# Kernel tuning notes

Measured on AMD Instinct MI355X. Metric: run time of the kernel, lower is better.

Reference implementation:

```python
import jax, jax.numpy as jnp
import numpy as np

N_IN = 1024
H = 16
N_QK = 64
N_V = 64
T = 2048
B = 2


def setup_inputs() -> dict:
    key = jax.random.key(0)
    ks = jax.random.split(key, 7)
    s = 1.0 / np.sqrt(N_IN)
    return {
        "x": jax.random.normal(ks[0], (T, B, N_IN), dtype=jnp.float32),
        "mask": jnp.ones((B, T), dtype=bool),
        "Wk": jax.random.normal(ks[1], (H * N_QK, N_IN), dtype=jnp.float32) * s,
        "bk": jax.random.normal(ks[2], (H * N_QK,), dtype=jnp.float32) * s,
        "Wq": jax.random.normal(ks[3], (H * N_QK, N_IN), dtype=jnp.float32) * s,
        "bq": jax.random.normal(ks[4], (H * N_QK,), dtype=jnp.float32) * s,
        "Wv": jax.random.normal(ks[5], (H * N_V, N_IN), dtype=jnp.float32) * s,
        "bv": jax.random.normal(ks[6], (H * N_V,), dtype=jnp.float32) * s,
    }


def reference(x, mask, Wk, bk, Wq, bq, Wv, bv):
    # x: (T, B, N_in); mask: (B, T) bool
    keys = (x @ Wk.T + bk).reshape(T, B, H, N_QK)      # (T,B,h,n_qk)
    queries = (x @ Wq.T + bq).reshape(T, B, H, N_QK)
    # kern[b,h,i,k] = keys_i . queries_k / sqrt(N_in)  (scale uses N_in, as in source)
    kern = jnp.einsum('ibhj,kbhj->bhik', keys, queries) / np.sqrt(N_IN)
    kern = jnp.where(mask[:, None, None, :], kern, -jnp.inf)
    A = jax.nn.softmax(kern, axis=-1)                  # softmax over last (query-index) axis
    values = (x @ Wv.T + bv).reshape(T, B, H, N_V)     # (T,B,h,n_v)
    out = jnp.einsum('bhij,jbhk->ibhk', A, values)     # (T,B,h,n_v)
    return out.reshape(T, B, H * N_V)
```

## Files before the change

kernel.cpp:

```cpp
#include <hip/hip_runtime.h>
#include <hip/hip_bf16.h>

#define TT 2048
#define BB 2
#define HH 16
#define DD 64
#define NIN 1024

#define KSCALE 0.0450842218f

using bf16x8 = __attribute__((ext_vector_type(8))) short;
using f32x4  = __attribute__((ext_vector_type(4))) float;
using f32x16 = __attribute__((ext_vector_type(16))) float;

__device__ __forceinline__ short f2b(float f) {
  union { float fl; unsigned u; } v; v.fl = f;
  return (short)((v.u + 0x7FFFu + ((v.u >> 16) & 1u)) >> 16);
}

__device__ __forceinline__ float exp2_fast(float x) {
  float r;
  asm("v_exp_f32 %0, %1" : "=v"(r) : "v"(x));
  return r;
}

__device__ __forceinline__ unsigned cvtpk(float lo, float hi) {
  unsigned r;
  asm("v_cvt_pk_bf16_f32 %0, %1, %2" : "=v"(r) : "v"(lo), "v"(hi));
  return r;
}

__device__ __forceinline__ void gld_lds16(const void* g, void* lds) {
  __builtin_amdgcn_global_load_lds(
      (const __attribute__((address_space(1))) void*)g,
      (__attribute__((address_space(3))) void*)lds, 16, 0, 0);
}

__global__ void cast_all_k(const float* __restrict__ x, const float* __restrict__ wk,
                           const float* __restrict__ wq, const float* __restrict__ wv,
                           short* __restrict__ xbf, short* __restrict__ wall) {
  int i = blockIdx.x * 256 + threadIdx.x;
  float4 v;
  short4* dp;
  float sc;
  if (i < 1048576) {
    v = reinterpret_cast<const float4*>(x)[i];
    dp = reinterpret_cast<short4*>(xbf) + i;
    sc = 1.0f;
  } else {
    int j = i - 1048576;
    int seg = j >> 18;
    const float* w = seg == 0 ? wk : (seg == 1 ? wq : wv);
    sc = (seg == 0) ? KSCALE : 1.0f;
    v = reinterpret_cast<const float4*>(w)[j & 262143];
    dp = reinterpret_cast<short4*>(wall) + j;
  }
  short4 o;
  o.x = f2b(v.x * sc);
  o.y = f2b(v.y * sc);
  o.z = f2b(v.z * sc);
  o.w = f2b(v.w * sc);
  *dp = o;
}

__device__ __forceinline__ int permc(int c) {
  return (c & 64) | ((c & 15) << 2) | ((c >> 4) & 3);
}

__global__ __launch_bounds__(256, 3)
void proj_gemm_k(const short* __restrict__ X, const short* __restrict__ Wall,
                 const float* __restrict__ bk, const float* __restrict__ bq,
                 const float* __restrict__ bv,
                 short* __restrict__ Kb, short* __restrict__ Qb, short* __restrict__ Vb) {
  __shared__ short As[128][64];
  __shared__ short Bs[128][64];
  const int tid = threadIdx.x;
  const int w = tid >> 6, l = tid & 63;
  const int bm = blockIdx.x, bn = blockIdx.y;
  const int wr = (w >> 1) * 64, wc = (w & 1) * 64;

  f32x4 acc[4][4] = {};
  const int sr = w * 8 + (l >> 3);

  for (int kt = 0; kt < NIN / 64; ++kt) {
    __syncthreads();
#pragma unroll
    for (int it = 0; it < 4; ++it) {
      int row = it * 32 + sr;
      int gc = ((l & 7) ^ (row & 7)) << 3;
      gld_lds16(X + (size_t)(bm * 128 + row) * NIN + kt * 64 + gc, &As[it * 32 + w * 8][0]);
      gld_lds16(Wall + (size_t)(bn * 128 + permc(row)) * NIN + kt * 64 + gc, &Bs[it * 32 + w * 8][0]);
    }
    __syncthreads();
#pragma unroll
    for (int kk = 0; kk < 2; ++kk) {
      bf16x8 af[4], bfr[4];
#pragma unroll
      for (int mf = 0; mf < 4; ++mf) {
        int row = wr + mf * 16 + (l & 15);
        af[mf] = *(const bf16x8*)&As[row][(kk * 32 + (l >> 4) * 8) ^ ((row & 7) << 3)];
      }
#pragma unroll
      for (int nf = 0; nf < 4; ++nf) {
        int row = wc + nf * 16 + (l & 15);
        bfr[nf] = *(const bf16x8*)&Bs[row][(kk * 32 + (l >> 4) * 8) ^ ((row & 7) << 3)];
      }
#pragma unroll
      for (int mf = 0; mf < 4; ++mf)
#pragma unroll
        for (int nf = 0; nf < 4; ++nf)
          acc[mf][nf] = __builtin_amdgcn_mfma_f32_16x16x32_bf16(af[mf], bfr[nf], acc[mf][nf], 0, 0, 0);
    }
  }

  const int seg = bn >> 3;
  const float* bp = (seg == 0) ? bk : (seg == 1) ? bq : bv;
  const float bscale = (seg == 0) ? KSCALE : 1.0f;

  const int dbase = ((l & 15) << 2);
  const int h = ((bn << 1) | (wc >> 6)) & 15;
  float bsc[4];
#pragma unroll
  for (int nf = 0; nf < 4; ++nf) bsc[nf] = bp[h * 64 + dbase + nf] * bscale;

  if (seg < 2) {
    short* dst = (seg == 0) ? Kb : Qb;
#pragma unroll
    for (int mf = 0; mf < 4; ++mf) {
#pragma unroll
      for (int r = 0; r < 4; ++r) {
        int m = bm * 128 + wr + mf * 16 + (l >> 4) * 4 + r;
        int t = m >> 1, b = m & 1;
        short4 o4;
        o4.x = f2b(acc[mf][0][r] + bsc[0]);
        o4.y = f2b(acc[mf][1][r] + bsc[1]);
        o4.z = f2b(acc[mf][2][r] + bsc[2]);
        o4.w = f2b(acc[mf][3][r] + bsc[3]);
        *(short4*)&dst[(((size_t)(b * HH + h)) * TT + t) * DD + dbase] = o4;
      }
    }
  } else {
#pragma unroll
    for (int mf = 0; mf < 4; ++mf) {
#pragma unroll
      for (int nf = 0; nf < 4; ++nf) {
        int d = dbase + nf;
#pragma unroll
        for (int r = 0; r < 4; ++r) {
          int m = bm * 128 + wr + mf * 16 + (l >> 4) * 4 + r;
          short ov = f2b(acc[mf][nf][r] + bsc[nf]);
          int t = m >> 1, b = m & 1;
          int tp = (t & ~12) | ((t & 4) << 1) | ((t & 8) >> 1);
          Vb[(((size_t)(b * HH + h)) * DD + d) * TT + tp] = ov;
        }
      }
    }
  }
}

__global__ __launch_bounds__(256, 2)
void attn_k(const short* __restrict__ Kb, const short* __restrict__ Qb,
            const short* __restrict__ Vt, float* __restrict__ out) {
  __shared__ short smem[16384];
  short* QsB = smem;
  short* VsB = smem + 8192;

  const int tid = threadIdx.x;
  const int w = tid >> 6, l = tid & 63;
  const int hi = l >> 5;

  const int fid = blockIdx.x;
  const int nf_id = (fid & 7) * 64 + (fid >> 3);
  const int ib = nf_id & 15;
  const int bh = nf_id >> 4;
  const size_t base = (size_t)bh * TT * DD;

  const int sr = w * 8 + (l >> 3);
  const int gsw = l & 7;

  bf16x8 kf[4];
  {
    const short* kp = Kb + base + (size_t)(ib * 128 + w * 32 + (l & 31)) * DD + hi * 8;
#pragma unroll
    for (int kd = 0; kd < 4; ++kd)
      kf[kd] = *(const bf16x8*)(kp + kd * 16);
  }

#pragma unroll
  for (int it = 0; it < 2; ++it) {
    int row = it * 32 + sr;
    int gc = (gsw ^ (row & 7)) << 3;
    gld_lds16(Qb + base + (size_t)row * DD + gc, QsB + (it * 32 + w * 8) * 64);
    gld_lds16(Vt + base + (size_t)row * TT + gc, VsB + (it * 32 + w * 8) * 64);
  }
  __syncthreads();

  f32x16 oacc[2] = {};
  float lsum_p = 0.f;

  for (int jt = 0; jt < TT / 64; ++jt) {
    const int cur = jt & 1;
    const short* Qs = QsB + cur * 4096;
    const short* Vs = VsB + cur * 4096;

    if (jt + 1 < TT / 64) {
#pragma unroll
      for (int it = 0; it < 2; ++it) {
        int row = it * 32 + sr;
        int gc = (gsw ^ (row & 7)) << 3;
        gld_lds16(Qb + base + (size_t)((jt + 1) * 64 + row) * DD + gc,
                  QsB + (cur ^ 1) * 4096 + (it * 32 + w * 8) * 64);
        gld_lds16(Vt + base + (size_t)row * TT + (jt + 1) * 64 + gc,
                  VsB + (cur ^ 1) * 4096 + (it * 32 + w * 8) * 64);
      }
    }

    f32x16 sacc[2] = {};
    __builtin_amdgcn_s_setprio(1);
#pragma unroll
    for (int js = 0; js < 2; ++js) {
      int qrow = js * 32 + (l & 31);
#pragma unroll
      for (int kd = 0; kd < 4; ++kd) {
        bf16x8 qf = *(const bf16x8*)&Qs[qrow * 64 + ((kd * 16 + hi * 8) ^ ((qrow & 7) << 3))];
        sacc[js] = __builtin_amdgcn_mfma_f32_32x32x16_bf16(qf, kf[kd], sacc[js], 0, 0, 0);
      }
    }
    __builtin_amdgcn_s_setprio(0);

#pragma unroll
    for (int js = 0; js < 2; ++js)
#pragma unroll
      for (int t = 0; t < 16; ++t)
        sacc[js][t] = exp2_fast(sacc[js][t]);

    {
      float tsum[16];
#pragma unroll
      for (int t = 0; t < 16; ++t) tsum[t] = sacc[0][t] + sacc[1][t];
#pragma unroll
      for (int st = 8; st > 0; st >>= 1)
#pragma unroll
        for (int t = 0; t < st; ++t) tsum[t] += tsum[t + st];
      lsum_p += tsum[0];
    }

#pragma unroll
    for (int kd4 = 0; kd4 < 4; ++kd4) {
      const int js = kd4 >> 1;
      const int r0 = (kd4 & 1) * 8;
      union { unsigned u[4]; bf16x8 v; } pu;
      pu.u[0] = cvtpk(sacc[js][r0 + 0], sacc[js][r0 + 1]);
      pu.u[1] = cvtpk(sacc[js][r0 + 2], sacc[js][r0 + 3]);
      pu.u[2] = cvtpk(sacc[js][r0 + 4], sacc[js][r0 + 5]);
      pu.u[3] = cvtpk(sacc[js][r0 + 6], sacc[js][r0 + 7]);
      __builtin_amdgcn_s_setprio(1);
#pragma unroll
      for (int ds = 0; ds < 2; ++ds) {
        int vrow = ds * 32 + (l & 31);
        bf16x8 vf = *(const bf16x8*)&Vs[vrow * 64 + ((kd4 * 16 + hi * 8) ^ ((vrow & 7) << 3))];
        oacc[ds] = __builtin_amdgcn_mfma_f32_32x32x16_bf16(vf, pu.v, oacc[ds], 0, 0, 0);
      }
      __builtin_amdgcn_s_setprio(0);
    }

    __syncthreads();
  }

  const int b = bh >> 4, h = bh & 15;
  const float lsum = lsum_p + __shfl_xor(lsum_p, 32, 64);
  const float invl = 1.0f / lsum;
  const int i = ib * 128 + w * 32 + (l & 31);
  float* orow = out + ((size_t)i * BB + b) * (HH * DD) + h * DD;
#pragma unroll
  for (int ds = 0; ds < 2; ++ds)
#pragma unroll
    for (int g = 0; g < 4; ++g) {
      float4 t;
      t.x = oacc[ds][4 * g + 0] * invl;
      t.y = oacc[ds][4 * g + 1] * invl;
      t.z = oacc[ds][4 * g + 2] * invl;
      t.w = oacc[ds][4 * g + 3] * invl;
      *(float4*)(orow + ds * 32 + g * 8 + 4 * hi) = t;
    }
}

extern "C" void kernel_launch(void* const* d_in, const int* in_sizes, int n_in,
                              void* d_out, int out_size, void* d_ws, size_t ws_size,
                              hipStream_t stream) {
  const float* x  = (const float*)d_in[0];
  const float* Wk = (const float*)d_in[2];
  const float* bk = (const float*)d_in[3];
  const float* Wq = (const float*)d_in[4];
  const float* bq = (const float*)d_in[5];
  const float* Wv = (const float*)d_in[6];
  const float* bv = (const float*)d_in[7];
  float* out = (float*)d_out;

  char* ws = (char*)d_ws;
  short* Xbf  = (short*)(ws + 0);
  short* Wall = (short*)(ws + 8388608);
  short* Kb   = (short*)(ws + 14680064);
  short* Qb   = (short*)(ws + 23068672);
  short* Vb   = (short*)(ws + 31457280);

  cast_all_k<<<7168, 256, 0, stream>>>(x, Wk, Wq, Wv, Xbf, Wall);

  dim3 pg(32, 24);
  proj_gemm_k<<<pg, 256, 0, stream>>>(Xbf, Wall, bk, bq, bv, Kb, Qb, Vb);

  attn_k<<<512, 256, 0, stream>>>(Kb, Qb, Vb, out);
}
```

Before: 84.45 us.

## Replace LDS-staged attention with single-wave blocks loading Q/V directly to registers

The attention kernel drops shared-memory staging and the block-wide barriers. It now launches 2048 single-wavefront blocks, each handling 32 rows. Q and V fragments are read straight from global memory into registers, with Q double-buffered across a two-step unrolled loop so the next tile's loads overlap the current tile's MFMAs. This removes LDS traffic and __syncthreads, but each wave now loads Q/V independently, so there is no sharing across the 4 waves and global/L2 traffic is roughly four times higher. V loads are issued in the same iteration they are consumed, which can expose latency.

```diff
diff --git a/kernel.cpp b/kernel.cpp
--- a/kernel.cpp
+++ b/kernel.cpp
@@ -158,119 +158,114 @@
   }
 }
 
-__global__ __launch_bounds__(256, 2)
+__global__ __launch_bounds__(64, 2)
 void attn_k(const short* __restrict__ Kb, const short* __restrict__ Qb,
             const short* __restrict__ Vt, float* __restrict__ out) {
-  __shared__ short smem[16384];
-  short* QsB = smem;
-  short* VsB = smem + 8192;
-
-  const int tid = threadIdx.x;
-  const int w = tid >> 6, l = tid & 63;
+  const int l = threadIdx.x & 63;
   const int hi = l >> 5;
 
   const int fid = blockIdx.x;
-  const int nf_id = (fid & 7) * 64 + (fid >> 3);
-  const int ib = nf_id & 15;
-  const int bh = nf_id >> 4;
+  const int nf_id = (fid & 7) * 256 + (fid >> 3);
+  const int ib = nf_id & 63;
+  const int bh = nf_id >> 6;
   const size_t base = (size_t)bh * TT * DD;
-
-  const int sr = w * 8 + (l >> 3);
-  const int gsw = l & 7;
 
   bf16x8 kf[4];
   {
-    const short* kp = Kb + base + (size_t)(ib * 128 + w * 32 + (l & 31)) * DD + hi * 8;
+    const short* kp = Kb + base + (size_t)(ib * 32 + (l & 31)) * DD + hi * 8;
 #pragma unroll
     for (int kd = 0; kd < 4; ++kd)
       kf[kd] = *(const bf16x8*)(kp + kd * 16);
   }
 
-#pragma unroll
-  for (int it = 0; it < 2; ++it) {
-    int row = it * 32 + sr;
-    int gc = (gsw ^ (row & 7)) << 3;
-    gld_lds16(Qb + base + (size_t)row * DD + gc, QsB + (it * 32 + w * 8) * 64);
-    gld_lds16(Vt + base + (size_t)row * TT + gc, VsB + (it * 32 + w * 8) * 64);
-  }
-  __syncthreads();
+  const short* qp = Qb + base + (size_t)(l & 31) * DD + hi * 8;
+  const short* vp = Vt + base + (size_t)(l & 31) * TT + hi * 8;
 
   f32x16 oacc[2] = {};
   float lsum_p = 0.f;
 
-  for (int jt = 0; jt < TT / 64; ++jt) {
-    const int cur = jt & 1;
-    const short* Qs = QsB + cur * 4096;
-    const short* Vs = VsB + cur * 4096;
-
-    if (jt + 1 < TT / 64) {
-#pragma unroll
-      for (int it = 0; it < 2; ++it) {
-        int row = it * 32 + sr;
-        int gc = (gsw ^ (row & 7)) << 3;
-        gld_lds16(Qb + base + (size_t)((jt + 1) * 64 + row) * DD + gc,
-                  QsB + (cur ^ 1) * 4096 + (it * 32 + w * 8) * 64);
-        gld_lds16(Vt + base + (size_t)row * TT + (jt + 1) * 64 + gc,
-                  VsB + (cur ^ 1) * 4096 + (it * 32 + w * 8) * 64);
-      }
-    }
-
-    f32x16 sacc[2] = {};
-    __builtin_amdgcn_s_setprio(1);
-#pragma unroll
-    for (int js = 0; js < 2; ++js) {
-      int qrow = js * 32 + (l & 31);
-#pragma unroll
-      for (int kd = 0; kd < 4; ++kd) {
-        bf16x8 qf = *(const bf16x8*)&Qs[qrow * 64 + ((kd * 16 + hi * 8) ^ ((qrow & 7) << 3))];
-        sacc[js] = __builtin_amdgcn_mfma_f32_32x32x16_bf16(qf, kf[kd], sacc[js], 0, 0, 0);
-      }
-    }
-    __builtin_amdgcn_s_setprio(0);
-
-#pragma unroll
-    for (int js = 0; js < 2; ++js)
-#pragma unroll
-      for (int t = 0; t < 16; ++t)
-        sacc[js][t] = exp2_fast(sacc[js][t]);
-
-    {
-      float tsum[16];
-#pragma unroll
-      for (int t = 0; t < 16; ++t) tsum[t] = sacc[0][t] + sacc[1][t];
-#pragma unroll
-      for (int st = 8; st > 0; st >>= 1)
-#pragma unroll
-        for (int t = 0; t < st; ++t) tsum[t] += tsum[t + st];
-      lsum_p += tsum[0];
-    }
-
-#pragma unroll
-    for (int kd4 = 0; kd4 < 4; ++kd4) {
-      const int js = kd4 >> 1;
-      const int r0 = (kd4 & 1) * 8;
-      union { unsigned u[4]; bf16x8 v; } pu;
-      pu.u[0] = cvtpk(sacc[js][r0 + 0], sacc[js][r0 + 1]);
-      pu.u[1] = cvtpk(sacc[js][r0 + 2], sacc[js][r0 + 3]);
-      pu.u[2] = cvtpk(sacc[js][r0 + 4], sacc[js][r0 + 5]);
-      pu.u[3] = cvtpk(sacc[js][r0 + 6], sacc[js][r0 + 7]);
-      __builtin_amdgcn_s_setprio(1);
-#pragma unroll
-      for (int ds = 0; ds < 2; ++ds) {
-        int vrow = ds * 32 + (l & 31);
-        bf16x8 vf = *(const bf16x8*)&Vs[vrow * 64 + ((kd4 * 16 + hi * 8) ^ ((vrow & 7) << 3))];
-        oacc[ds] = __builtin_amdgcn_mfma_f32_32x32x16_bf16(vf, pu.v, oacc[ds], 0, 0, 0);
-      }
-      __builtin_amdgcn_s_setprio(0);
-    }
-
-    __syncthreads();
-  }
+  bf16x8 qfA[8], qfB[8];
+#pragma unroll
+  for (int js = 0; js < 2; ++js)
+#pragma unroll
+    for (int kd = 0; kd < 4; ++kd)
+      qfA[js * 4 + kd] = *(const bf16x8*)(qp + js * 2048 + kd * 16);
+
+#define ATTN_BODY(QC, QN, JT)                                                   \
+  {                                                                             \
+               \
+    bf16x8 vf[8];                                                               \
+    _Pragma("unroll")                                                           \
+    for (int ds = 0; ds < 2; ++ds)                                              \
+      _Pragma("unroll")                                                         \
+      for (int kd4 = 0; kd4 < 4; ++kd4)                                         \
+        vf[ds * 4 + kd4] = *(const bf16x8*)(vp + ds * 65536 + kd4 * 16);        \
+    vp += 64;                                                                   \
+               \
+    if ((JT) + 1 < TT / 64) {                                                   \
+      qp += 4096;                                                               \
+      _Pragma("unroll")                                                         \
+      for (int js = 0; js < 2; ++js)                                            \
+        _Pragma("unroll")                                                       \
+        for (int kd = 0; kd < 4; ++kd)                                          \
+          QN[js * 4 + kd] = *(const bf16x8*)(qp + js * 2048 + kd * 16);         \
+    }                                                                           \
+            \
+    f32x16 sacc[2] = {};                                                        \
+    __builtin_amdgcn_s_setprio(1);                                              \
+    _Pragma("unroll")                                                           \
+    for (int js = 0; js < 2; ++js)                                              \
+      _Pragma("unroll")                                                         \
+      for (int kd = 0; kd < 4; ++kd)                                            \
+        sacc[js] = __builtin_amdgcn_mfma_f32_32x32x16_bf16(QC[js * 4 + kd],     \
+                                                           kf[kd], sacc[js], 0, 0, 0); \
+    __builtin_amdgcn_s_setprio(0);                                              \
+                                                      \
+    _Pragma("unroll")                                                           \
+    for (int js = 0; js < 2; ++js)                                              \
+      _Pragma("unroll")                                                         \
+      for (int t = 0; t < 16; ++t)                                              \
+        sacc[js][t] = exp2_fast(sacc[js][t]);                                   \
+                                  \
+    {                                                                           \
+      float tsum[16];                                                           \
+      _Pragma("unroll")                                                         \
+      for (int t = 0; t < 16; ++t) tsum[t] = sacc[0][t] + sacc[1][t];           \
+      _Pragma("unroll")                                                         \
+      for (int st = 8; st > 0; st >>= 1)                                        \
+        _Pragma("unroll")                                                       \
+        for (int t = 0; t < st; ++t) tsum[t] += tsum[t + st];                   \
+      lsum_p += tsum[0];                                                        \
+    }                                                                           \
+                   \
+    _Pragma("unroll")                                                           \
+    for (int kd4 = 0; kd4 < 4; ++kd4) {                                         \
+      const int js = kd4 >> 1;                                                  \
+      const int r0 = (kd4 & 1) * 8;                                             \
+      union { unsigned u[4]; bf16x8 v; } pu;                                    \
+      pu.u[0] = cvtpk(sacc[js][r0 + 0], sacc[js][r0 + 1]);                      \
+      pu.u[1] = cvtpk(sacc[js][r0 + 2], sacc[js][r0 + 3]);                      \
+      pu.u[2] = cvtpk(sacc[js][r0 + 4], sacc[js][r0 + 5]);                      \
+      pu.u[3] = cvtpk(sacc[js][r0 + 6], sacc[js][r0 + 7]);                      \
+      __builtin_amdgcn_s_setprio(1);                                            \
+      _Pragma("unroll")                                                         \
+      for (int ds = 0; ds < 2; ++ds)                                            \
+        oacc[ds] = __builtin_amdgcn_mfma_f32_32x32x16_bf16(vf[ds * 4 + kd4],    \
+                                                           pu.v, oacc[ds], 0, 0, 0); \
+      __builtin_amdgcn_s_setprio(0);                                            \
+    }                                                                           \
+  }
+
+  for (int jt = 0; jt < TT / 64; jt += 2) {
+    ATTN_BODY(qfA, qfB, jt);
+    ATTN_BODY(qfB, qfA, jt + 1);
+  }
+#undef ATTN_BODY
 
   const int b = bh >> 4, h = bh & 15;
   const float lsum = lsum_p + __shfl_xor(lsum_p, 32, 64);
   const float invl = 1.0f / lsum;
-  const int i = ib * 128 + w * 32 + (l & 31);
+  const int i = ib * 32 + (l & 31);
   float* orow = out + ((size_t)i * BB + b) * (HH * DD) + h * DD;
 #pragma unroll
   for (int ds = 0; ds < 2; ++ds)
@@ -309,5 +304,5 @@
   dim3 pg(32, 24);
   proj_gemm_k<<<pg, 256, 0, stream>>>(Xbf, Wall, bk, bq, bv, Kb, Qb, Vb);
 
-  attn_k<<<512, 256, 0, stream>>>(Kb, Qb, Vb, out);
-}
+  attn_k<<<2048, 64, 0, stream>>>(Kb, Qb, Vb, out);
+}
```

New measurement: 156.9 us. 1.86x slower.

## Restructure attention into single-wave blocks each owning 64 key rows

Applied to the files above, without the earlier changes.

The attention kernel changes from 256-thread blocks (4 waves, 32 rows each) to 64-thread single-wave blocks that each handle 64 rows via two 32-row MFMA tiles sharing every Q/V LDS fragment load. Block barriers are replaced by vmcnt waits since only one wave touches the LDS buffers, and the grid doubles to 1024 blocks. This aims to cut LDS reads per MFMA and barrier overhead. In exchange each wave loads the whole tile into LDS itself, register pressure roughly doubles for the accumulators, and each workgroup still reserves 32KB of LDS for a single wave, which limits waves per CU.

```diff
diff --git a/kernel.cpp b/kernel.cpp
--- a/kernel.cpp
+++ b/kernel.cpp
@@ -158,45 +158,44 @@
   }
 }
 
-__global__ __launch_bounds__(256, 2)
+__global__ __launch_bounds__(64, 1)
 void attn_k(const short* __restrict__ Kb, const short* __restrict__ Qb,
             const short* __restrict__ Vt, float* __restrict__ out) {
   __shared__ short smem[16384];
   short* QsB = smem;
   short* VsB = smem + 8192;
 
-  const int tid = threadIdx.x;
-  const int w = tid >> 6, l = tid & 63;
+  const int l = threadIdx.x & 63;
   const int hi = l >> 5;
 
   const int fid = blockIdx.x;
-  const int nf_id = (fid & 7) * 64 + (fid >> 3);
-  const int ib = nf_id & 15;
-  const int bh = nf_id >> 4;
+  const int nf_id = (fid & 7) * 128 + (fid >> 3);
+  const int ib = nf_id & 31;
+  const int bh = nf_id >> 5;
   const size_t base = (size_t)bh * TT * DD;
 
-  const int sr = w * 8 + (l >> 3);
-  const int gsw = l & 7;
-
-  bf16x8 kf[4];
-  {
-    const short* kp = Kb + base + (size_t)(ib * 128 + w * 32 + (l & 31)) * DD + hi * 8;
+  const int srow = l >> 3;
+  const int gcol = ((l & 7) ^ (srow & 7)) << 3;
+
+  bf16x8 kf[2][4];
+#pragma unroll
+  for (int i = 0; i < 2; ++i) {
+    const short* kp = Kb + base + (size_t)(ib * 64 + i * 32 + (l & 31)) * DD + hi * 8;
 #pragma unroll
     for (int kd = 0; kd < 4; ++kd)
-      kf[kd] = *(const bf16x8*)(kp + kd * 16);
-  }
-
-#pragma unroll
-  for (int it = 0; it < 2; ++it) {
-    int row = it * 32 + sr;
-    int gc = (gsw ^ (row & 7)) << 3;
-    gld_lds16(Qb + base + (size_t)row * DD + gc, QsB + (it * 32 + w * 8) * 64);
-    gld_lds16(Vt + base + (size_t)row * TT + gc, VsB + (it * 32 + w * 8) * 64);
-  }
-  __syncthreads();
-
-  f32x16 oacc[2] = {};
-  float lsum_p = 0.f;
+      kf[i][kd] = *(const bf16x8*)(kp + kd * 16);
+  }
+
+#pragma unroll
+  for (int it = 0; it < 8; ++it) {
+    gld_lds16(Qb + base + (size_t)(it * 8 + srow) * DD + gcol, QsB + it * 512);
+    gld_lds16(Vt + base + (size_t)(it * 8 + srow) * TT + gcol, VsB + it * 512);
+  }
+  asm volatile("s_waitcnt vmcnt(0)" ::: "memory");
+  __builtin_amdgcn_sched_barrier(0);
+
+  f32x16 oacc[2][2] = {};
+  float lsum_p[2] = {0.f, 0.f};
 
   for (int jt = 0; jt < TT / 64; ++jt) {
     const int cur = jt & 1;
@@ -205,84 +204,93 @@
 
     if (jt + 1 < TT / 64) {
 #pragma unroll
-      for (int it = 0; it < 2; ++it) {
-        int row = it * 32 + sr;
-        int gc = (gsw ^ (row & 7)) << 3;
-        gld_lds16(Qb + base + (size_t)((jt + 1) * 64 + row) * DD + gc,
-                  QsB + (cur ^ 1) * 4096 + (it * 32 + w * 8) * 64);
-        gld_lds16(Vt + base + (size_t)row * TT + (jt + 1) * 64 + gc,
-                  VsB + (cur ^ 1) * 4096 + (it * 32 + w * 8) * 64);
-      }
-    }
-
-    f32x16 sacc[2] = {};
+      for (int it = 0; it < 8; ++it) {
+        gld_lds16(Qb + base + (size_t)((jt + 1) * 64 + it * 8 + srow) * DD + gcol,
+                  QsB + (cur ^ 1) * 4096 + it * 512);
+        gld_lds16(Vt + base + (size_t)(it * 8 + srow) * TT + (jt + 1) * 64 + gcol,
+                  VsB + (cur ^ 1) * 4096 + it * 512);
+      }
+    }
+
+    f32x16 sacc[2][2] = {};
     __builtin_amdgcn_s_setprio(1);
 #pragma unroll
-    for (int js = 0; js < 2; ++js) {
-      int qrow = js * 32 + (l & 31);
-#pragma unroll
-      for (int kd = 0; kd < 4; ++kd) {
+    for (int kd = 0; kd < 4; ++kd) {
+#pragma unroll
+      for (int js = 0; js < 2; ++js) {
+        int qrow = js * 32 + (l & 31);
         bf16x8 qf = *(const bf16x8*)&Qs[qrow * 64 + ((kd * 16 + hi * 8) ^ ((qrow & 7) << 3))];
-        sacc[js] = __builtin_amdgcn_mfma_f32_32x32x16_bf16(qf, kf[kd], sacc[js], 0, 0, 0);
+        sacc[0][js] = __builtin_amdgcn_mfma_f32_32x32x16_bf16(qf, kf[0][kd], sacc[0][js], 0, 0, 0);
+        sacc[1][js] = __builtin_amdgcn_mfma_f32_32x32x16_bf16(qf, kf[1][kd], sacc[1][js], 0, 0, 0);
       }
     }
     __builtin_amdgcn_s_setprio(0);
 
-#pragma unroll
-    for (int js = 0; js < 2; ++js)
-#pragma unroll
-      for (int t = 0; t < 16; ++t)
-        sacc[js][t] = exp2_fast(sacc[js][t]);
-
-    {
+    bf16x8 pu[2][4];
+#pragma unroll
+    for (int i = 0; i < 2; ++i) {
+#pragma unroll
+      for (int js = 0; js < 2; ++js)
+#pragma unroll
+        for (int t = 0; t < 16; ++t)
+          sacc[i][js][t] = exp2_fast(sacc[i][js][t]);
       float tsum[16];
 #pragma unroll
-      for (int t = 0; t < 16; ++t) tsum[t] = sacc[0][t] + sacc[1][t];
+      for (int t = 0; t < 16; ++t) tsum[t] = sacc[i][0][t] + sacc[i][1][t];
 #pragma unroll
       for (int st = 8; st > 0; st >>= 1)
 #pragma unroll
         for (int t = 0; t < st; ++t) tsum[t] += tsum[t + st];
-      lsum_p += tsum[0];
+      lsum_p[i] += tsum[0];
+#pragma unroll
+      for (int kd4 = 0; kd4 < 4; ++kd4) {
+        const int js = kd4 >> 1;
+        const int r0 = (kd4 & 1) * 8;
+        union { unsigned u[4]; bf16x8 v; } t;
+        t.u[0] = cvtpk(sacc[i][js][r0 + 0], sacc[i][js][r0 + 1]);
+        t.u[1] = cvtpk(sacc[i][js][r0 + 2], sacc[i][js][r0 + 3]);
+        t.u[2] = cvtpk(sacc[i][js][r0 + 4], sacc[i][js][r0 + 5]);
+        t.u[3] = cvtpk(sacc[i][js][r0 + 6], sacc[i][js][r0 + 7]);
+        pu[i][kd4] = t.v;
+      }
     }
 
 #pragma unroll
     for (int kd4 = 0; kd4 < 4; ++kd4) {
-      const int js = kd4 >> 1;
-      const int r0 = (kd4 & 1) * 8;
-      union { unsigned u[4]; bf16x8 v; } pu;
-      pu.u[0] = cvtpk(sacc[js][r0 + 0], sacc[js][r0 + 1]);
-      pu.u[1] = cvtpk(sacc[js][r0 + 2], sacc[js][r0 + 3]);
-      pu.u[2] = cvtpk(sacc[js][r0 + 4], sacc[js][r0 + 5]);
-      pu.u[3] = cvtpk(sacc[js][r0 + 6], sacc[js][r0 + 7]);
       __builtin_amdgcn_s_setprio(1);
 #pragma unroll
       for (int ds = 0; ds < 2; ++ds) {
         int vrow = ds * 32 + (l & 31);
         bf16x8 vf = *(const bf16x8*)&Vs[vrow * 64 + ((kd4 * 16 + hi * 8) ^ ((vrow & 7) << 3))];
-        oacc[ds] = __builtin_amdgcn_mfma_f32_32x32x16_bf16(vf, pu.v, oacc[ds], 0, 0, 0);
+        oacc[0][ds] = __builtin_amdgcn_mfma_f32_32x32x16_bf16(vf, pu[0][kd4], oacc[0][ds], 0, 0, 0);
+        oacc[1][ds] = __builtin_amdgcn_mfma_f32_32x32x16_bf16(vf, pu[1][kd4], oacc[1][ds], 0, 0, 0);
       }
       __builtin_amdgcn_s_setprio(0);
     }
 
-    __syncthreads();
+    asm volatile("s_waitcnt vmcnt(0)" ::: "memory");
+    __builtin_amdgcn_sched_barrier(0);
   }
 
   const int b = bh >> 4, h = bh & 15;
-  const float lsum = lsum_p + __shfl_xor(lsum_p, 32, 64);
-  const float invl = 1.0f / lsum;
-  const int i = ib * 128 + w * 32 + (l & 31);
-  float* orow = out + ((size_t)i * BB + b) * (HH * DD) + h * DD;
-#pragma unroll
-  for (int ds = 0; ds < 2; ++ds)
-#pragma unroll
-    for (int g = 0; g < 4; ++g) {
-      float4 t;
-      t.x = oacc[ds][4 * g + 0] * invl;
-      t.y = oacc[ds][4 * g + 1] * invl;
-      t.z = oacc[ds][4 * g + 2] * invl;
-      t.w = oacc[ds][4 * g + 3] * invl;
-      *(float4*)(orow + ds * 32 + g * 8 + 4 * hi) = t;
-    }
+#pragma unroll
+  for (int i = 0; i < 2; ++i) {
+    const float lsum = lsum_p[i] + __shfl_xor(lsum_p[i], 32, 64);
+    const float invl = 1.0f / lsum;
+    const int irow = ib * 64 + i * 32 + (l & 31);
+    float* orow = out + ((size_t)irow * BB + b) * (HH * DD) + h * DD;
+#pragma unroll
+    for (int ds = 0; ds < 2; ++ds)
+#pragma unroll
+      for (int g = 0; g < 4; ++g) {
+        float4 t;
+        t.x = oacc[i][ds][4 * g + 0] * invl;
+        t.y = oacc[i][ds][4 * g + 1] * invl;
+        t.z = oacc[i][ds][4 * g + 2] * invl;
+        t.w = oacc[i][ds][4 * g + 3] * invl;
+        *(float4*)(orow + ds * 32 + g * 8 + 4 * hi) = t;
+      }
+  }
 }
 
 extern "C" void kernel_launch(void* const* d_in, const int* in_sizes, int n_in,
@@ -309,5 +317,5 @@
   dim3 pg(32, 24);
   proj_gemm_k<<<pg, 256, 0, stream>>>(Xbf, Wall, bk, bq, bv, Kb, Qb, Vb);
 
-  attn_k<<<512, 256, 0, stream>>>(Kb, Qb, Vb, out);
-}
+  attn_k<<<1024, 64, 0, stream>>>(Kb, Qb, Vb, out);
+}
```

Result: slower. 97.12 us (+15.0%).

## Triple-buffer Q/V tiles in attention with prefetch depth two and partial waitcnt

Applied to the files above, without the earlier changes.

Switches the attention kernel's Q and V shared-memory staging from double to triple buffering, prefetching tile jt+2 while computing tile jt. Full __syncthreads is replaced with an explicit vmcnt(4) wait plus s_barrier, so one tile's loads stay in flight across the barrier. The aim is to hide global-to-LDS load latency better. LDS use per block grows from 32KB to 48KB, which could limit occupancy alongside the 2-block launch bound.

```diff
diff --git a/kernel.cpp b/kernel.cpp
--- a/kernel.cpp
+++ b/kernel.cpp
@@ -161,9 +161,9 @@
 __global__ __launch_bounds__(256, 2)
 void attn_k(const short* __restrict__ Kb, const short* __restrict__ Qb,
             const short* __restrict__ Vt, float* __restrict__ out) {
-  __shared__ short smem[16384];
+  __shared__ short smem[24576];
   short* QsB = smem;
-  short* VsB = smem + 8192;
+  short* VsB = smem + 12288;
 
   const int tid = threadIdx.x;
   const int w = tid >> 6, l = tid & 63;
@@ -186,34 +186,35 @@
       kf[kd] = *(const bf16x8*)(kp + kd * 16);
   }
 
-#pragma unroll
-  for (int it = 0; it < 2; ++it) {
-    int row = it * 32 + sr;
-    int gc = (gsw ^ (row & 7)) << 3;
-    gld_lds16(Qb + base + (size_t)row * DD + gc, QsB + (it * 32 + w * 8) * 64);
-    gld_lds16(Vt + base + (size_t)row * TT + gc, VsB + (it * 32 + w * 8) * 64);
-  }
-  __syncthreads();
+#define STAGE(TILE, BK)                                                          \
+  {                                                                              \
+    _Pragma("unroll")                                                            \
+    for (int it = 0; it < 2; ++it) {                                             \
+      int row = it * 32 + sr;                                                    \
+      int gc = (gsw ^ (row & 7)) << 3;                                           \
+      gld_lds16(Qb + base + (size_t)((TILE) * 64 + row) * DD + gc,               \
+                QsB + (BK) * 4096 + (it * 32 + w * 8) * 64);                     \
+      gld_lds16(Vt + base + (size_t)row * TT + (TILE) * 64 + gc,                 \
+                VsB + (BK) * 4096 + (it * 32 + w * 8) * 64);                     \
+    }                                                                            \
+  }
+
+  STAGE(0, 0);
+  STAGE(1, 1);
+  asm volatile("s_waitcnt vmcnt(4)" ::: "memory");
+  __builtin_amdgcn_s_barrier();
+  __builtin_amdgcn_sched_barrier(0);
 
   f32x16 oacc[2] = {};
   float lsum_p = 0.f;
 
+  int bc = 0;
   for (int jt = 0; jt < TT / 64; ++jt) {
-    const int cur = jt & 1;
-    const short* Qs = QsB + cur * 4096;
-    const short* Vs = VsB + cur * 4096;
-
-    if (jt + 1 < TT / 64) {
-#pragma unroll
-      for (int it = 0; it < 2; ++it) {
-        int row = it * 32 + sr;
-        int gc = (gsw ^ (row & 7)) << 3;
-        gld_lds16(Qb + base + (size_t)((jt + 1) * 64 + row) * DD + gc,
-                  QsB + (cur ^ 1) * 4096 + (it * 32 + w * 8) * 64);
-        gld_lds16(Vt + base + (size_t)row * TT + (jt + 1) * 64 + gc,
-                  VsB + (cur ^ 1) * 4096 + (it * 32 + w * 8) * 64);
-      }
-    }
+    int b2 = bc + 2; if (b2 >= 3) b2 -= 3;
+    const short* Qs = QsB + bc * 4096;
+    const short* Vs = VsB + bc * 4096;
+
+    if (jt + 2 < TT / 64) STAGE(jt + 2, b2);
 
     f32x16 sacc[2] = {};
     __builtin_amdgcn_s_setprio(1);
@@ -264,8 +265,16 @@
       __builtin_amdgcn_s_setprio(0);
     }
 
-    __syncthreads();
-  }
+    if (jt + 2 < TT / 64)
+      asm volatile("s_waitcnt vmcnt(4)" ::: "memory");
+    else
+      asm volatile("s_waitcnt vmcnt(0)" ::: "memory");
+    __builtin_amdgcn_s_barrier();
+    __builtin_amdgcn_sched_barrier(0);
+
+    bc = (bc + 1 == 3) ? 0 : bc + 1;
+  }
+#undef STAGE
 
   const int b = bh >> 4, h = bh & 15;
   const float lsum = lsum_p + __shfl_xor(lsum_p, 32, 64);
```

New measurement: 85.62 us. No clear change (+1.4%).
